# Kernel tuning notes

Hardware: AMD Instinct MI355X
Metric: run time of the kernel (lower is better)

## Reference

```python
import jax, jax.numpy as jnp
import numpy as np

B, CIN, H, W = 4, 272, 32, 32
D, NHEAD, DFF, E, TOPK, NDEC = 256, 8, 1024, 8, 2, 2
HW = H * W


def _sine_pos():
    npf = D // 2
    ye = jnp.cumsum(jnp.ones((H, W), jnp.float32), 0)
    xe = jnp.cumsum(jnp.ones((H, W), jnp.float32), 1)
    eps, scale = 1e-6, 2.0 * np.pi
    ye = ye / (ye[-1:, :] + eps) * scale
    xe = xe / (xe[:, -1:] + eps) * scale
    t = jnp.arange(npf, dtype=jnp.float32)
    dim_t = 10000.0 ** (2.0 * jnp.floor(t / 2.0) / npf)
    px = xe[:, :, None] / dim_t
    py = ye[:, :, None] / dim_t
    px = jnp.stack((jnp.sin(px[:, :, 0::2]), jnp.cos(px[:, :, 1::2])), axis=3).reshape(H, W, npf)
    py = jnp.stack((jnp.sin(py[:, :, 0::2]), jnp.cos(py[:, :, 1::2])), axis=3).reshape(H, W, npf)
    return jnp.concatenate((py, px), axis=2).reshape(HW, D)


def _ln(v, g, b):
    m = v.mean(-1, keepdims=True)
    var = ((v - m) ** 2).mean(-1, keepdims=True)
    return (v - m) / jnp.sqrt(var + 1e-5) * g + b


def _mha(q_in, k_in, v_in, Wqkv, bqkv, Wo, bo):
    # seq-first [S,B,D], torch nn.MultiheadAttention math (dropout off)
    S = q_in.shape[0]; T = k_in.shape[0]; dh = D // NHEAD
    Wq, Wk, Wv = jnp.split(Wqkv, 3, 0)
    bq, bk, bv = jnp.split(bqkv, 3)
    q = (q_in @ Wq.T + bq).reshape(S, B, NHEAD, dh)
    k = (k_in @ Wk.T + bk).reshape(T, B, NHEAD, dh)
    v = (v_in @ Wv.T + bv).reshape(T, B, NHEAD, dh)
    attn = jax.nn.softmax(jnp.einsum('sbhd,tbhd->bhst', q, k) / np.sqrt(dh), axis=-1)
    o = jnp.einsum('bhst,tbhd->sbhd', attn, v).reshape(S, B, D)
    return o @ Wo.T + bo


def _moe(xt, Wg, bg, W1, b1, W2, b2):
    # FMoETransformerMLP with NaiveGate: top-k gate, per-expert 2-layer MLP, weighted combine
    S = xt.shape[0]
    xf = xt.reshape(-1, D)
    N = xf.shape[0]
    logits = xf @ Wg.T + bg                              # [N, E]
    topv, topi = jax.lax.top_k(logits, TOPK)             # [N, k]
    score = jax.nn.softmax(topv, axis=-1)                # softmax over selected logits
    comb = jnp.zeros((N, E), xf.dtype).at[jnp.arange(N)[:, None], topi].add(score)
    h = jax.nn.relu(jnp.einsum('nd,edh->neh', xf, W1) + b1)   # [N, E, DFF]
    y = jnp.einsum('neh,ehd->ned', h, W2) + b2                # [N, E, D]
    out = jnp.einsum('ne,ned->nd', comb, y)
    return out.reshape(S, B, D)


def setup_inputs() -> dict:
    key = jax.random.key(0)
    ks = iter(jax.random.split(key, 32))
    g = lambda shp, s=0.02: s * jax.random.normal(next(ks), shp, jnp.float32)
    inp = {
        'x': jax.random.normal(next(ks), (B, CIN, H, W), jnp.float32),
        'Wi': g((D, CIN)), 'bi': jnp.zeros((D,), jnp.float32),
        'learned_embed': g((HW, D), 1.0),
        'Wqkv_s': g((3 * D, D)), 'bqkv_s': jnp.zeros((3 * D,), jnp.float32),
        'Wo_s': g((D, D)), 'bo_s': jnp.zeros((D,), jnp.float32),
        'Wqkv_c': g((3 * D, D)), 'bqkv_c': jnp.zeros((3 * D,), jnp.float32),
        'Wo_c': g((D, D)), 'bo_c': jnp.zeros((D,), jnp.float32),
        'ln_g': jnp.ones((4 * NDEC, D), jnp.float32), 'ln_b': jnp.zeros((4 * NDEC, D), jnp.float32),
        'gate_w1': g((E, D)), 'gate_b1': jnp.zeros((E,), jnp.float32),
        'W1a': g((E, D, DFF)), 'b1a': jnp.zeros((E, DFF), jnp.float32),
        'W2a': g((E, DFF, D)), 'b2a': jnp.zeros((E, D), jnp.float32),
        'gate_w2': g((E, D)), 'gate_b2': jnp.zeros((E,), jnp.float32),
        'W1b': g((E, D, DFF)), 'b1b': jnp.zeros((E, DFF), jnp.float32),
        'W2b': g((E, DFF, D)), 'b2b': jnp.zeros((E, D), jnp.float32),
        'Wout': g((CIN, D)), 'bout': jnp.zeros((CIN,), jnp.float32),
    }
    return inp


def reference(x, Wi, bi, learned_embed, Wqkv_s, bqkv_s, Wo_s, bo_s,
              Wqkv_c, bqkv_c, Wo_c, bo_c, ln_g, ln_b,
              gate_w1, gate_b1, W1a, b1a, W2a, b2a,
              gate_w2, gate_b2, W1b, b1b, W2b, b2b, Wout, bout):
    tokens = x.transpose(2, 3, 0, 1).reshape(HW, B, CIN)   # 'b c h w -> (h w) b c'
    src = tokens @ Wi.T + bi                               # input_proj
    pos = _sine_pos()[:, None, :]                          # [HW,1,D] broadcast over batch
    enc = src
    dec = src
    for i in range(NDEC):
        tgt = jnp.broadcast_to(learned_embed[:, None, :], (HW, B, D))
        t2 = _mha(tgt + pos, enc + pos, enc, Wqkv_s, bqkv_s, Wo_s, bo_s)
        tgt = _ln(tgt + t2, ln_g[4 * i], ln_b[4 * i])
        t2 = _mha(tgt + pos, dec + pos, dec, Wqkv_c, bqkv_c, Wo_c, bo_c)
        tgt = _ln(tgt + t2, ln_g[4 * i + 1], ln_b[4 * i + 1])
        od = tgt + _moe(tgt, gate_w1, gate_b1, W1a, b1a, W2a, b2a)   # post-lnorm: residual only
        od = _ln(od, ln_g[4 * i + 2], ln_b[4 * i + 2])
        od = od + _moe(od, gate_w2, gate_b2, W1b, b1b, W2b, b2b)
        dec = _ln(od, ln_g[4 * i + 3], ln_b[4 * i + 3])
    rec = dec @ Wout.T + bout                              # output_proj, [HW,B,CIN]
    feature_rec = rec.reshape(H, W, B, CIN).transpose(2, 3, 0, 1)
    return feature_rec
```

## Files before the change

kernel.cpp:

```cpp
#include <hip/hip_runtime.h>

#define NHW 1024
#define NB 4
#define DM 256
#define NTOK 4096
#define NCIN 272
#define NDFF 1024

typedef unsigned short u16;
typedef unsigned int u32;
typedef __attribute__((ext_vector_type(8))) short s16x8;
typedef __attribute__((ext_vector_type(4))) float f32x4;

static const int GEMM_SMEM32 = (32+32+64+64)*56*2;
static const int GEMM_SMEM64 = (32+32+64+64)*72*2;

__device__ __forceinline__ float4 ld4(const float* p){ return *(const float4*)p; }
__device__ __forceinline__ void st4(float* p, float4 v){ *(float4*)p = v; }

__device__ __forceinline__ void splitf(float x, u16& h, u16& l){
  u32 u = __float_as_uint(x);
  u32 hu = (u + (0x7FFFu + ((u >> 16) & 1u))) >> 16;
  h = (u16)hu;
  float hf = __uint_as_float(hu << 16);
  float r = x - hf;
  u32 v = __float_as_uint(r);
  v += 0x7FFFu + ((v >> 16) & 1u);
  l = (u16)(v >> 16);
}

__device__ __forceinline__ u32 packf(float x){
  u16 h,l; splitf(x,h,l);
  return (u32)h | ((u32)l << 16);
}

__global__ void pos_kernel(float* __restrict__ pos){
  int s = blockIdx.x, d = threadIdx.x;
  int row = s >> 5, col = s & 31;
  float base = (d < 128) ? (float)(row + 1) : (float)(col + 1);
  float val = base / (32.0f + 1e-6f) * 6.2831853071795864f;
  int dd = (d < 128) ? d : d - 128;
  int mf = dd >> 1;
  float f = powf(10000.0f, (float)mf * (1.0f/64.0f));
  float a = val / f;
  pos[s*DM + d] = (dd & 1) ? cosf(a) : sinf(a);
}

__global__ void tin_kernel(const float* __restrict__ x, float* __restrict__ tok){
  int idx = blockIdx.x*256 + threadIdx.x;
  if (idx >= NTOK*NCIN) return;
  int c = idx % NCIN;
  int n = idx / NCIN;
  int s = n >> 2, b = n & 3;
  tok[idx] = x[((long)(b*NCIN + c))*NHW + s];
}
__global__ void tout_kernel(const float* __restrict__ rec, float* __restrict__ out){
  int idx = blockIdx.x*256 + threadIdx.x;
  if (idx >= NTOK*NCIN) return;
  int s = idx & (NHW-1);
  int bc = idx >> 10;
  int b = bc / NCIN, c = bc % NCIN;
  out[idx] = rec[((long)(s*NB + b))*NCIN + c];
}

__global__ __launch_bounds__(256) void tconv_kernel(const float* __restrict__ in,
    u16* __restrict__ oh, u16* __restrict__ ol, int K, int N){
  __shared__ float tile[32][33];
  long base = (long)blockIdx.z * (long)K * (long)N;
  int k0 = blockIdx.y*32, n0 = blockIdx.x*32;
  int tx = threadIdx.x & 31, ty = threadIdx.x >> 5;
  #pragma unroll
  for (int i=0;i<32;i+=8)
    tile[ty+i][tx] = in[base + (long)(k0+ty+i)*N + n0+tx];
  __syncthreads();
  #pragma unroll
  for (int i=0;i<32;i+=8){
    float v = tile[tx][ty+i];
    u16 h,l; splitf(v,h,l);
    long o = base + (long)(n0+ty+i)*K + k0+tx;
    oh[o]=h; ol[o]=l;
  }
}

__global__ void wsplit_kernel(const float* __restrict__ in, u16* __restrict__ oh,
    u16* __restrict__ ol, int n){
  int i = blockIdx.x*256 + threadIdx.x;
  if (i < n){ u16 h,l; splitf(in[i],h,l); oh[i]=h; ol[i]=l; }
}

template<bool GROUPED, bool INDIRECT, int ASRC, bool RELU, int CDST, int BK>
__device__ __forceinline__ void sgemm_body(
    const void* __restrict__ Av, int lda,
    const float* __restrict__ pos,
    const u16* __restrict__ Bhp, const u16* __restrict__ Blp, int ldb,
    const float* __restrict__ bias,
    void* __restrict__ Cv, int ldc,
    int M, int N, int K,
    const int* __restrict__ map,
    const int* __restrict__ cnt,
    const int* __restrict__ offs,
    const int* __restrict__ jmap,
    const float* __restrict__ sflat,
    long strideB, int strideBias, int e)
{
  constexpr int BM = 32;
  constexpr int NSEG = BK/32;
  constexpr int SW = (BK==32) ? 56 : 72;
  int rows = GROUPED ? cnt[e] : M;
  int bn = blockIdx.x, bm = blockIdx.y;
  if (bm*BM >= rows) return;
  int row0 = GROUPED ? offs[e] : 0;
  const float* Af = (const float*)Av;
  const u32*   Ap = (const u32*)Av;
  if (GROUPED){ Bhp += (long)e*strideB; Blp += (long)e*strideB; }
  const float* biasp = bias ? (GROUPED ? bias + (long)e*strideBias : bias) : nullptr;

  extern __shared__ u16 smem[];
  u16* Ah = smem;
  u16* Al = Ah + BM*SW;
  u16* Bh = Al + BM*SW;
  u16* Bl = Bh + 64*SW;

  int tid = threadIdx.x;
  int w = tid >> 6, ln = tid & 63;
  int wm = w >> 1, wn = w & 1;
  int lr = ln & 15, lh = ln >> 4;
  int srow = tid >> 2, sseg = tid & 3;

  int bgrow = bn*64 + srow;
  bool bok = bgrow < N;
  int agrow = bm*BM + srow;
  bool aok = (tid < BM*4) && (agrow < rows);
  long arow = 0;
  if (aok) arow = INDIRECT ? (long)map[row0 + agrow] : (long)(row0 + agrow);

  const f32x4 z4 = {0.f,0.f,0.f,0.f};
  f32x4 acc0 = z4, acc1 = z4;
  const s16x8 z8 = {0,0,0,0,0,0,0,0};

  s16x8 rBh[NSEG], rBl[NSEG];
  uint4 rA0[NSEG], rA1[NSEG];
  float4 rP0[NSEG], rP1[NSEG];

  auto load_stage = [&](int k0){
    #pragma unroll
    for (int s=0; s<NSEG; s++){
      int kk = k0 + s*32 + sseg*8;
      bool kok = kk < K;
      rBh[s] = z8; rBl[s] = z8;
      if (bok && kok){
        rBh[s] = *(const s16x8*)&Bhp[(long)bgrow*ldb + kk];
        rBl[s] = *(const s16x8*)&Blp[(long)bgrow*ldb + kk];
      }
      if (tid < BM*4){
        rA0[s] = make_uint4(0,0,0,0); rA1[s] = make_uint4(0,0,0,0);
        if (ASRC==2 || ASRC==3){ rP0[s] = make_float4(0.f,0.f,0.f,0.f); rP1[s] = rP0[s]; }
        if (aok && kok){
          if (ASRC == 1){
            rA0[s] = *(const uint4*)&Ap[arow*lda + kk];
            rA1[s] = *(const uint4*)&Ap[arow*lda + kk + 4];
          } else {
            long aoff = (ASRC==3 ? (long)(arow>>2) : arow)*lda + kk;
            rA0[s] = *(const uint4*)&Af[aoff];
            rA1[s] = *(const uint4*)&Af[aoff + 4];
            if (ASRC==2 || ASRC==3){
              long poff = (long)(arow>>2)*DM + kk;
              rP0[s] = ld4(&pos[poff]);
              rP1[s] = ld4(&pos[poff + 4]);
            }
          }
        }
      }
    }
  };

  auto write_stage = [&](){
    #pragma unroll
    for (int s=0; s<NSEG; s++){
      *(s16x8*)&Bh[srow*SW + s*32 + sseg*8] = rBh[s];
      *(s16x8*)&Bl[srow*SW + s*32 + sseg*8] = rBl[s];
      if (tid < BM*4){
        s16x8 hv, lv;
        if (ASRC == 1){
          u32 ws[8] = {rA0[s].x,rA0[s].y,rA0[s].z,rA0[s].w,rA1[s].x,rA1[s].y,rA1[s].z,rA1[s].w};
          #pragma unroll
          for (int t=0;t<8;t++){ hv[t]=(short)(ws[t]&0xFFFFu); lv[t]=(short)(ws[t]>>16); }
        } else {
          float xs[8] = {__uint_as_float(rA0[s].x),__uint_as_float(rA0[s].y),
                         __uint_as_float(rA0[s].z),__uint_as_float(rA0[s].w),
                         __uint_as_float(rA1[s].x),__uint_as_float(rA1[s].y),
                         __uint_as_float(rA1[s].z),__uint_as_float(rA1[s].w)};
          if (ASRC==2 || ASRC==3){
            xs[0]+=rP0[s].x; xs[1]+=rP0[s].y; xs[2]+=rP0[s].z; xs[3]+=rP0[s].w;
            xs[4]+=rP1[s].x; xs[5]+=rP1[s].y; xs[6]+=rP1[s].z; xs[7]+=rP1[s].w;
          }
          #pragma unroll
          for (int t=0;t<8;t++){ u16 hh,ll; splitf(xs[t],hh,ll); hv[t]=(short)hh; lv[t]=(short)ll; }
        }
        *(s16x8*)&Ah[srow*SW + s*32 + sseg*8] = hv;
        *(s16x8*)&Al[srow*SW + s*32 + sseg*8] = lv;
      }
    }
  };

  load_stage(0);
  for (int k0 = 0; k0 < K; k0 += BK){
    write_stage();
    __syncthreads();
    if (k0 + BK < K) load_stage(k0 + BK);
    #pragma unroll
    for (int s=0; s<NSEG; s++){
      int co = s*32 + lh*8;
      s16x8 a0h = *(const s16x8*)&Ah[(wm*16 + lr)*SW + co];
      s16x8 a0l = *(const s16x8*)&Al[(wm*16 + lr)*SW + co];
      s16x8 b0h = *(const s16x8*)&Bh[(wn*32      + lr)*SW + co];
      s16x8 b1h = *(const s16x8*)&Bh[(wn*32 + 16 + lr)*SW + co];
      s16x8 b0l = *(const s16x8*)&Bl[(wn*32      + lr)*SW + co];
      s16x8 b1l = *(const s16x8*)&Bl[(wn*32 + 16 + lr)*SW + co];
      acc0 = __builtin_amdgcn_mfma_f32_16x16x32_bf16(a0h, b0h, acc0, 0,0,0);
      acc1 = __builtin_amdgcn_mfma_f32_16x16x32_bf16(a0h, b1h, acc1, 0,0,0);
      acc0 = __builtin_amdgcn_mfma_f32_16x16x32_bf16(a0h, b0l, acc0, 0,0,0);
      acc1 = __builtin_amdgcn_mfma_f32_16x16x32_bf16(a0h, b1l, acc1, 0,0,0);
      acc0 = __builtin_amdgcn_mfma_f32_16x16x32_bf16(a0l, b0h, acc0, 0,0,0);
      acc1 = __builtin_amdgcn_mfma_f32_16x16x32_bf16(a0l, b1h, acc1, 0,0,0);
    }
    __syncthreads();
  }

  int c0 = bn*64 + wn*32 + lr;
  int c1 = c0 + 16;
  float bv0 = (biasp && c0 < N) ? biasp[c0] : 0.f;
  float bv1 = (biasp && c1 < N) ? biasp[c1] : 0.f;
  int rbase = bm*BM + wm*16 + lh*4;
  auto stc = [&](int gr, int gc, float vv){
    if (gr < rows && gc < N){
      float t = RELU ? fmaxf(vv, 0.f) : vv;
      if (CDST == 1){
        ((u32*)Cv)[(long)(row0+gr)*ldc + gc] = packf(t);
      } else if (CDST == 2){
        int ts = jmap[row0+gr];
        ((float*)Cv)[(long)ts*ldc + gc] = t * sflat[ts];
      } else {
        ((float*)Cv)[(long)(row0+gr)*ldc + gc] = t;
      }
    }
  };
  #pragma unroll
  for (int r = 0; r < 4; r++){
    stc(rbase + r, c0, acc0[r] + bv0);
    stc(rbase + r, c1, acc1[r] + bv1);
  }
}

__global__ __launch_bounds__(256) void gemm_in(const float* A, const u16* Bh_, const u16* Bl_,
    const float* bias, float* C){
  sgemm_body<false,false,0,false,0,32>(A, NCIN, nullptr, Bh_, Bl_, NCIN, bias, C, DM,
      NTOK, DM, NCIN, nullptr, nullptr, nullptr, nullptr, nullptr, 0, 0, 0);
}

__global__ __launch_bounds__(256) void gemm_out_k(const float* A, const u16* Bh_, const u16* Bl_,
    const float* bias, float* C){
  sgemm_body<false,false,0,false,0,32>(A, DM, nullptr, Bh_, Bl_, DM, bias, C, NCIN,
      NTOK, NCIN, DM, nullptr, nullptr, nullptr, nullptr, nullptr, 0, 0, 0);
}

__global__ __launch_bounds__(256) void gemm_wos(const u32* A, const u16* Bh_, const u16* Bl_,
    const float* bias, float* C){
  sgemm_body<false,false,1,false,0,32>(A, DM, nullptr, Bh_, Bl_, DM, bias, C, DM,
      NTOK, DM, DM, nullptr, nullptr, nullptr, nullptr, nullptr, 0, 0, 0);
}

__global__ __launch_bounds__(256) void gemm_woc(const u32* A, const u16* Bh_, const u16* Bl_,
    const float* bias, float* C){
  sgemm_body<false,false,1,false,0,32>(A, DM, nullptr, Bh_, Bl_, DM, bias, C, DM,
      NTOK, DM, DM, nullptr, nullptr, nullptr, nullptr, nullptr, 0, 0, 0);
}

template<int MQ, int MK>
__device__ __forceinline__ void qkv_body(const float* Aq, const float* Ak, const float* Avv,
    const float* pos, const u16* Bwh, const u16* Bwl, const float* bias,
    u32* Cq, u32* Ck, u32* Cvv){
  int z = blockIdx.z;
  const float* A = z==0 ? Aq : (z==1 ? Ak : Avv);
  u32* C = z==0 ? Cq : (z==1 ? Ck : Cvv);
  const u16* Bph = Bwh + (long)z*256*DM;
  const u16* Bpl = Bwl + (long)z*256*DM;
  const float* bp = bias + z*256;
  int mode = z==0 ? MQ : (z==1 ? MK : 0);
  if (mode == 3)
    sgemm_body<false,false,3,false,1,32>(A, DM, pos, Bph, Bpl, DM, bp, C, DM,
        NTOK, DM, DM, nullptr, nullptr, nullptr, nullptr, nullptr, 0, 0, 0);
  else if (mode == 2)
    sgemm_body<false,false,2,false,1,32>(A, DM, pos, Bph, Bpl, DM, bp, C, DM,
        NTOK, DM, DM, nullptr, nullptr, nullptr, nullptr, nullptr, 0, 0, 0);
  else
    sgemm_body<false,false,0,false,1,32>(A, DM, pos, Bph, Bpl, DM, bp, C, DM,
        NTOK, DM, DM, nullptr, nullptr, nullptr, nullptr, nullptr, 0, 0, 0);
}

__global__ __launch_bounds__(256) void gemm_qkv_s(const float* Aq, const float* Ak,
    const float* Avv, const float* pos, const u16* Bwh, const u16* Bwl, const float* bias,
    u32* Cq, u32* Ck, u32* Cvv){
  qkv_body<3,2>(Aq, Ak, Avv, pos, Bwh, Bwl, bias, Cq, Ck, Cvv);
}
__global__ __launch_bounds__(256) void gemm_qkv_c(const float* Aq, const float* Ak,
    const float* Avv, const float* pos, const u16* Bwh, const u16* Bwl, const float* bias,
    u32* Cq, u32* Ck, u32* Cvv){
  qkv_body<2,2>(Aq, Ak, Avv, pos, Bwh, Bwl, bias, Cq, Ck, Cvv);
}

__global__ __launch_bounds__(256) void gemm_m1(const float* A, const u16* Bh_, const u16* Bl_,
    const float* bias, u32* C, const int* map, const int* cnt, const int* offs){
  sgemm_body<true,true,0,true,1,32>(A, DM, nullptr, Bh_, Bl_, DM, bias, C, NDFF,
      0, NDFF, DM, map, cnt, offs, nullptr, nullptr, 262144L, NDFF, blockIdx.z);
}

__global__ __launch_bounds__(256) void gemm_m2(const u32* A, const u16* Bh_, const u16* Bl_,
    const float* bias, float* C, const int* cnt, const int* offs,
    const int* jmap, const float* sflat){
  sgemm_body<true,false,1,false,2,64>(A, NDFF, nullptr, Bh_, Bl_, NDFF, bias, C, DM,
      0, DM, NDFF, nullptr, cnt, offs, jmap, sflat, 262144L, DM, blockIdx.z);
}

__global__ __launch_bounds__(256) void attn_mfma(const u32* __restrict__ Q,
    const u32* __restrict__ Kb, const u32* __restrict__ Vb, u32* __restrict__ O)
{
  __shared__ u16 Kh[64*40], Kl[64*40];
  __shared__ u16 Vh[32*72], Vl[32*72];
  __shared__ u16 Ph[4][16*72], Pl[4][16*72];

  int qt = blockIdx.x, bh = blockIdx.y;
  int b = bh >> 3, h = bh & 7;
  int tid = threadIdx.x;
  int wv = tid >> 6, ln = tid & 63;
  int lr = ln & 15, lh = ln >> 4;
  const float scale = 0.17677669529663687f;

  s16x8 qh, ql;
  {
    long qrow = ((long)((qt*64 + wv*16 + lr)*NB + b))*DM + h*32 + lh*8;
    uint4 p0 = *(const uint4*)&Q[qrow];
    uint4 p1 = *(const uint4*)&Q[qrow + 4];
    u32 ws[8] = {p0.x,p0.y,p0.z,p0.w,p1.x,p1.y,p1.z,p1.w};
    #pragma unroll
    for (int t=0;t<8;t++){ qh[t]=(short)(ws[t]&0xFFFFu); ql[t]=(short)(ws[t]>>16); }
  }

  int skey = tid >> 2, soct = tid & 3;
  int vkey0 = tid >> 3,        vd0 = (tid & 7) << 2;
  int vkey1 = (tid + 256) >> 3, vd1 = ((tid + 256) & 7) << 2;

  uint4 rK0, rK1, rV0, rV1;

  auto load_kv = [&](int kt){
    long gk = ((long)((kt*64 + skey)*NB + b))*DM + h*32 + soct*8;
    rK0 = *(const uint4*)&Kb[gk];
    rK1 = *(const uint4*)&Kb[gk + 4];
    rV0 = *(const uint4*)&Vb[((long)((kt*64 + vkey0)*NB + b))*DM + h*32 + vd0];
    rV1 = *(const uint4*)&Vb[((long)((kt*64 + vkey1)*NB + b))*DM + h*32 + vd1];
  };

  auto write_kv = [&](){
    u32 ws[8] = {rK0.x,rK0.y,rK0.z,rK0.w,rK1.x,rK1.y,rK1.z,rK1.w};
    s16x8 hv, lv;
    #pragma unroll
    for (int t=0;t<8;t++){ hv[t]=(short)(ws[t]&0xFFFFu); lv[t]=(short)(ws[t]>>16); }
    *(s16x8*)&Kh[skey*40 + soct*8] = hv;
    *(s16x8*)&Kl[skey*40 + soct*8] = lv;
    u32 v0[4] = {rV0.x,rV0.y,rV0.z,rV0.w};
    u32 v1[4] = {rV1.x,rV1.y,rV1.z,rV1.w};
    #pragma unroll
    for (int t=0;t<4;t++){
      Vh[(vd0+t)*72 + vkey0] = (u16)(v0[t]&0xFFFFu);
      Vl[(vd0+t)*72 + vkey0] = (u16)(v0[t]>>16);
      Vh[(vd1+t)*72 + vkey1] = (u16)(v1[t]&0xFFFFu);
      Vl[(vd1+t)*72 + vkey1] = (u16)(v1[t]>>16);
    }
  };

  const f32x4 z4 = {0.f,0.f,0.f,0.f};
  f32x4 oacc0 = z4, oacc1 = z4;
  float m[4]  = {-1e30f,-1e30f,-1e30f,-1e30f};
  float lp[4] = {0.f,0.f,0.f,0.f};

  load_kv(0);
  for (int kt = 0; kt < 16; kt++){
    write_kv();
    __syncthreads();
    if (kt + 1 < 16) load_kv(kt + 1);

    f32x4 sacc[4];
    #pragma unroll
    for (int s16t=0; s16t<4; s16t++){
      s16x8 kbh = *(const s16x8*)&Kh[(s16t*16 + lr)*40 + lh*8];
      s16x8 kbl = *(const s16x8*)&Kl[(s16t*16 + lr)*40 + lh*8];
      f32x4 a = z4;
      a = __builtin_amdgcn_mfma_f32_16x16x32_bf16(qh, kbh, a, 0,0,0);
      a = __builtin_amdgcn_mfma_f32_16x16x32_bf16(qh, kbl, a, 0,0,0);
      a = __builtin_amdgcn_mfma_f32_16x16x32_bf16(ql, kbh, a, 0,0,0);
      a[0]*=scale; a[1]*=scale; a[2]*=scale; a[3]*=scale;
      sacc[s16t] = a;
    }
    float tm[4];
    #pragma unroll
    for (int r=0;r<4;r++)
      tm[r] = fmaxf(fmaxf(sacc[0][r],sacc[1][r]), fmaxf(sacc[2][r],sacc[3][r]));
    #pragma unroll
    for (int mask=1; mask<=8; mask<<=1){
      #pragma unroll
      for (int r=0;r<4;r++) tm[r] = fmaxf(tm[r], __shfl_xor(tm[r], mask));
    }
    #pragma unroll
    for (int r=0;r<4;r++){
      float mn = fmaxf(m[r], tm[r]);
      float al = __expf(m[r] - mn);
      m[r] = mn;
      lp[r] *= al;
      oacc0[r] *= al;
      oacc1[r] *= al;
    }
    #pragma unroll
    for (int s16t=0; s16t<4; s16t++){
      #pragma unroll
      for (int r=0;r<4;r++){
        float p = __expf(sacc[s16t][r] - m[r]);
        lp[r] += p;
        u16 hh,ll; splitf(p,hh,ll);
        int off = (lh*4 + r)*72 + s16t*16 + lr;
        Ph[wv][off] = hh;
        Pl[wv][off] = ll;
      }
    }
    #pragma unroll
    for (int ks=0; ks<2; ks++){
      s16x8 pah = *(const s16x8*)&Ph[wv][lr*72 + ks*32 + lh*8];
      s16x8 pal = *(const s16x8*)&Pl[wv][lr*72 + ks*32 + lh*8];
      s16x8 vh0 = *(const s16x8*)&Vh[lr*72      + ks*32 + lh*8];
      s16x8 vl0 = *(const s16x8*)&Vl[lr*72      + ks*32 + lh*8];
      s16x8 vh1 = *(const s16x8*)&Vh[(16+lr)*72 + ks*32 + lh*8];
      s16x8 vl1 = *(const s16x8*)&Vl[(16+lr)*72 + ks*32 + lh*8];
      oacc0 = __builtin_amdgcn_mfma_f32_16x16x32_bf16(pah, vh0, oacc0, 0,0,0);
      oacc0 = __builtin_amdgcn_mfma_f32_16x16x32_bf16(pah, vl0, oacc0, 0,0,0);
      oacc0 = __builtin_amdgcn_mfma_f32_16x16x32_bf16(pal, vh0, oacc0, 0,0,0);
      oacc1 = __builtin_amdgcn_mfma_f32_16x16x32_bf16(pah, vh1, oacc1, 0,0,0);
      oacc1 = __builtin_amdgcn_mfma_f32_16x16x32_bf16(pah, vl1, oacc1, 0,0,0);
      oacc1 = __builtin_amdgcn_mfma_f32_16x16x32_bf16(pal, vh1, oacc1, 0,0,0);
    }
    __syncthreads();
  }
  #pragma unroll
  for (int mask=1; mask<=8; mask<<=1){
    #pragma unroll
    for (int r=0;r<4;r++) lp[r] += __shfl_xor(lp[r], mask);
  }
  #pragma unroll
  for (int r=0;r<4;r++){
    float inv = 1.f/lp[r];
    int q = qt*64 + wv*16 + lh*4 + r;
    long orow = ((long)(q*NB + b))*DM + h*32;
    O[orow + lr]      = packf(oacc0[r]*inv);
    O[orow + 16 + lr] = packf(oacc1[r]*inv);
  }
}

__device__ __forceinline__ float wave_sum(float v){
  #pragma unroll
  for (int m=1; m<64; m<<=1) v += __shfl_xor(v, m);
  return v;
}

__device__ __forceinline__ float4 ln_finish(float4 a, const float* g, const float* beta, int lane){
  float sum = wave_sum(a.x+a.y+a.z+a.w);
  float sq  = wave_sum(a.x*a.x + a.y*a.y + a.z*a.z + a.w*a.w);
  float mean = sum * (1.f/DM);
  float var  = sq * (1.f/DM) - mean*mean;
  float inv = 1.0f / sqrtf(var + 1e-5f);
  float4 gg = ld4(&g[lane*4]);
  float4 bb = ld4(&beta[lane*4]);
  float4 ov;
  ov.x = (a.x-mean)*inv*gg.x + bb.x;
  ov.y = (a.y-mean)*inv*gg.y + bb.y;
  ov.z = (a.z-mean)*inv*gg.z + bb.z;
  ov.w = (a.w-mean)*inv*gg.w + bb.w;
  return ov;
}

__device__ __forceinline__ void gate_from_regs(float4 ov, int row, int lane,
    const float* GW, const float* GB, float* scores, int* topi){
  float lg[8];
  #pragma unroll
  for (int e=0; e<8; e++){
    float4 wv = ld4(&GW[e*DM + lane*4]);
    lg[e] = ov.x*wv.x + ov.y*wv.y + ov.z*wv.z + ov.w*wv.w;
  }
  #pragma unroll
  for (int mask=1; mask<64; mask<<=1){
    #pragma unroll
    for (int e=0; e<8; e++) lg[e] += __shfl_xor(lg[e], mask);
  }
  #pragma unroll
  for (int e=0; e<8; e++) lg[e] += GB[e];
  int i0 = 0; float v0 = lg[0];
  #pragma unroll
  for (int e=1; e<8; e++) if (lg[e] > v0){ v0 = lg[e]; i0 = e; }
  int i1 = -1; float v1 = -1e30f;
  #pragma unroll
  for (int e=0; e<8; e++) if (e != i0 && lg[e] > v1){ v1 = lg[e]; i1 = e; }
  if (lane == 0){
    float ee = expf(v1 - v0);
    float inv = 1.f/(1.f + ee);
    scores[row*2]   = inv;
    scores[row*2+1] = ee*inv;
    topi[row*2]   = i0;
    topi[row*2+1] = i1;
  }
}

__global__ __launch_bounds__(256) void add_ln_le(const float* __restrict__ A,
    const float* __restrict__ Bv, const float* __restrict__ g, const float* __restrict__ beta,
    float* __restrict__ out)
{
  int row = blockIdx.x*4 + (threadIdx.x >> 6);
  int lane = threadIdx.x & 63;
  float4 a = ld4(&A[(long)(row>>2)*DM + lane*4]);
  float4 b = ld4(&Bv[(long)row*DM + lane*4]);
  a.x+=b.x; a.y+=b.y; a.z+=b.z; a.w+=b.w;
  float4 ov = ln_finish(a, g, beta, lane);
  st4(&out[(long)row*DM + lane*4], ov);
}

__global__ __launch_bounds__(256) void add_ln_gate(const float* __restrict__ A,
    const float* __restrict__ Bv, const float* __restrict__ g, const float* __restrict__ beta,
    float* __restrict__ out, const float* __restrict__ GW, const float* __restrict__ GB,
    float* __restrict__ scores, int* __restrict__ topi)
{
  int row = blockIdx.x*4 + (threadIdx.x >> 6);
  int lane = threadIdx.x & 63;
  float4 a = ld4(&A[(long)row*DM + lane*4]);
  float4 b = ld4(&Bv[(long)row*DM + lane*4]);
  a.x+=b.x; a.y+=b.y; a.z+=b.z; a.w+=b.w;
  float4 ov = ln_finish(a, g, beta, lane);
  st4(&out[(long)row*DM + lane*4], ov);
  gate_from_regs(ov, row, lane, GW, GB, scores, topi);
}

__global__ __launch_bounds__(256) void moe_ln_gate_k(const float* __restrict__ base,
    const float* __restrict__ yt,
    const float* __restrict__ g, const float* __restrict__ beta, float* __restrict__ out,
    const float* __restrict__ GW, const float* __restrict__ GB,
    float* __restrict__ scores2, int* __restrict__ topi2)
{
  int row = blockIdx.x*4 + (threadIdx.x >> 6);
  int lane = threadIdx.x & 63;
  float4 a  = ld4(&base[(long)row*DM + lane*4]);
  float4 y0 = ld4(&yt[(long)(row*2)*DM + lane*4]);
  float4 y1 = ld4(&yt[(long)(row*2+1)*DM + lane*4]);
  a.x += y0.x + y1.x;
  a.y += y0.y + y1.y;
  a.z += y0.z + y1.z;
  a.w += y0.w + y1.w;
  float4 ov = ln_finish(a, g, beta, lane);
  st4(&out[(long)row*DM + lane*4], ov);
  gate_from_regs(ov, row, lane, GW, GB, scores2, topi2);
}

__global__ __launch_bounds__(256) void moe_ln_fin_k(const float* __restrict__ base,
    const float* __restrict__ yt,
    const float* __restrict__ g, const float* __restrict__ beta, float* __restrict__ out)
{
  int row = blockIdx.x*4 + (threadIdx.x >> 6);
  int lane = threadIdx.x & 63;
  float4 a  = ld4(&base[(long)row*DM + lane*4]);
  float4 y0 = ld4(&yt[(long)(row*2)*DM + lane*4]);
  float4 y1 = ld4(&yt[(long)(row*2+1)*DM + lane*4]);
  a.x += y0.x + y1.x;
  a.y += y0.y + y1.y;
  a.z += y0.z + y1.z;
  a.w += y0.w + y1.w;
  float4 ov = ln_finish(a, g, beta, lane);
  st4(&out[(long)row*DM + lane*4], ov);
}

__global__ void offs_assign(const int* __restrict__ topi, int* __restrict__ cnt_g,
    int* __restrict__ offs_g, int* __restrict__ map, int* __restrict__ jmap)
{
  __shared__ int hist[72];
  __shared__ int offs[8];
  __shared__ int c2[8];
  int tid = threadIdx.x;
  if (tid < 72) hist[tid] = 0;
  __syncthreads();
  for (int idx = tid; idx < 2*NTOK; idx += 256){
    int e = topi[idx];
    atomicAdd(&hist[e*9 + (tid & 7)], 1);
  }
  __syncthreads();
  if (tid == 0){
    int o = 0;
    #pragma unroll
    for (int e=0; e<8; e++){
      int c = 0;
      #pragma unroll
      for (int s=0; s<8; s++) c += hist[e*9 + s];
      cnt_g[e] = c;
      offs[e] = o;
      offs_g[e] = o;
      o += c;
      c2[e] = 0;
    }
  }
  __syncthreads();
  for (int n = tid; n < NTOK; n += 256){
    #pragma unroll
    for (int j=0; j<2; j++){
      int e = topi[n*2+j];
      int slot = atomicAdd(&c2[e], 1);
      int r = offs[e] + slot;
      map[r] = n;
      jmap[r] = n*2 + j;
    }
  }
}

extern "C" void kernel_launch(void* const* d_in, const int* in_sizes, int n_in,
                              void* d_out, int out_size, void* d_ws, size_t ws_size,
                              hipStream_t stream)
{
  const float* x      = (const float*)d_in[0];
  const float* Wi     = (const float*)d_in[1];
  const float* bi     = (const float*)d_in[2];
  const float* le     = (const float*)d_in[3];
  const float* Wqkv_s = (const float*)d_in[4];
  const float* bqkv_s = (const float*)d_in[5];
  const float* Wo_s   = (const float*)d_in[6];
  const float* bo_s   = (const float*)d_in[7];
  const float* Wqkv_c = (const float*)d_in[8];
  const float* bqkv_c = (const float*)d_in[9];
  const float* Wo_c   = (const float*)d_in[10];
  const float* bo_c   = (const float*)d_in[11];
  const float* ln_g   = (const float*)d_in[12];
  const float* ln_b   = (const float*)d_in[13];
  const float* gw1    = (const float*)d_in[14];
  const float* gb1    = (const float*)d_in[15];
  const float* W1a    = (const float*)d_in[16];
  const float* b1a    = (const float*)d_in[17];
  const float* W2a    = (const float*)d_in[18];
  const float* b2a    = (const float*)d_in[19];
  const float* gw2    = (const float*)d_in[20];
  const float* gb2    = (const float*)d_in[21];
  const float* W1b    = (const float*)d_in[22];
  const float* b1b    = (const float*)d_in[23];
  const float* W2b    = (const float*)d_in[24];
  const float* b2b    = (const float*)d_in[25];
  const float* Wout   = (const float*)d_in[26];
  const float* bout   = (const float*)d_in[27];

  float* w = (float*)d_ws;
  const long SZ = 1048576;
  float* pos  = w;
  float* src  = pos  + 262144;
  float* t2s  = src  + SZ;
  float* tgtA = t2s  + SZ;
  float* dec  = tgtA + SZ;
  float* od   = dec;
  float* od2  = dec  + SZ;
  float* yt   = od2  + SZ;
  float* scoresA = yt + 2097152;
  float* scoresB = scoresA + 8192;
  u16* wsp  = (u16*)(scoresB + 8192);
  u16* W1ah = wsp;             u16* W1al = wsp + 2097152;
  u16* W1bh = wsp + 4194304;   u16* W1bl = wsp + 6291456;
  u16* W2ah = wsp + 8388608;   u16* W2al = wsp + 10485760;
  u16* W2bh = wsp + 12582912;  u16* W2bl = wsp + 14680064;
  u16* dwp  = wsp + 16777216;
  u16* Wih   = dwp;            u16* Wil   = dwp + 69632;
  u16* Wqsh  = dwp + 139264;   u16* Wqsl  = dwp + 335872;
  u16* Wosh  = dwp + 532480;   u16* Wosl  = dwp + 598016;
  u16* Wqch  = dwp + 663552;   u16* Wqcl  = dwp + 860160;
  u16* Woch  = dwp + 1056768;  u16* Wocl  = dwp + 1122304;
  u16* Wouth = dwp + 1187840;  u16* Woutl = dwp + 1257472;
  float* R   = (float*)(dwp + 1327104);
  float* tok = R;
  u32*  q    = (u32*)R;
  u32*  k    = (u32*)(R + SZ);
  u32*  v    = (u32*)(R + 2*SZ);
  u32*  ao   = (u32*)(R + 3*SZ);
  u32*  hg   = (u32*)R;
  float* rec = R;
  int* ip    = (int*)(R + 8388608);
  int* topiA = ip;
  int* topiB = ip + 8192;
  int* map   = ip + 16384;
  int* jmapA = ip + 24576;
  int* jmapB = ip + 32768;
  int* cnts  = ip + 40960;
  int* offsg = ip + 40992;

  dim3 blk(256);
  dim3 gDense(4, 128, 1);
  dim3 gQKV(4, 128, 3);
  dim3 gMoe1(16, 128, 8);
  dim3 gMoe2(4, 128, 8);
  dim3 gAttn(16, 32);

  pos_kernel<<<NHW, DM, 0, stream>>>(pos);
  tin_kernel<<<(NTOK*NCIN + 255)/256, blk, 0, stream>>>(x, tok);

  tconv_kernel<<<dim3(32, 8, 8), blk, 0, stream>>>(W1a, W1ah, W1al, DM,   NDFF);
  tconv_kernel<<<dim3(32, 8, 8), blk, 0, stream>>>(W1b, W1bh, W1bl, DM,   NDFF);
  tconv_kernel<<<dim3(8, 32, 8), blk, 0, stream>>>(W2a, W2ah, W2al, NDFF, DM);
  tconv_kernel<<<dim3(8, 32, 8), blk, 0, stream>>>(W2b, W2bh, W2bl, NDFF, DM);
  wsplit_kernel<<<272, blk, 0, stream>>>(Wi,     Wih,   Wil,   69632);
  wsplit_kernel<<<768, blk, 0, stream>>>(Wqkv_s, Wqsh,  Wqsl,  196608);
  wsplit_kernel<<<256, blk, 0, stream>>>(Wo_s,   Wosh,  Wosl,  65536);
  wsplit_kernel<<<768, blk, 0, stream>>>(Wqkv_c, Wqch,  Wqcl,  196608);
  wsplit_kernel<<<256, blk, 0, stream>>>(Wo_c,   Woch,  Wocl,  65536);
  wsplit_kernel<<<272, blk, 0, stream>>>(Wout,   Wouth, Woutl, 69632);

  gemm_in<<<gDense, blk, GEMM_SMEM32, stream>>>(tok, Wih, Wil, bi, src);

  gemm_qkv_s<<<gQKV, blk, GEMM_SMEM32, stream>>>(le, src, src, pos, Wqsh, Wqsl, bqkv_s, q, k, v);
  attn_mfma<<<gAttn, blk, 0, stream>>>(q, k, v, ao);
  gemm_wos<<<gDense, blk, GEMM_SMEM32, stream>>>(ao, Wosh, Wosl, bo_s, t2s);

  const float* decIn = src;
  for (int i = 0; i < 2; i++){
    int* cntA = cnts + (i*2)*8;   int* offsA = offsg + (i*2)*8;
    int* cntB = cnts + (i*2+1)*8; int* offsB = offsg + (i*2+1)*8;

    add_ln_le<<<1024, blk, 0, stream>>>(le, t2s, ln_g + (4*i)*DM, ln_b + (4*i)*DM, tgtA);
    gemm_qkv_c<<<gQKV, blk, GEMM_SMEM32, stream>>>(tgtA, decIn, decIn, pos, Wqch, Wqcl, bqkv_c, q, k, v);
    attn_mfma<<<gAttn, blk, 0, stream>>>(q, k, v, ao);
    gemm_woc<<<gDense, blk, GEMM_SMEM32, stream>>>(ao, Woch, Wocl, bo_c, (float*)k);
    add_ln_gate<<<1024, blk, 0, stream>>>(tgtA, (float*)k, ln_g + (4*i+1)*DM, ln_b + (4*i+1)*DM, od,
        gw1, gb1, scoresA, topiA);

    offs_assign<<<1, blk, 0, stream>>>(topiA, cntA, offsA, map, jmapA);
    gemm_m1<<<gMoe1, blk, GEMM_SMEM32, stream>>>(od, W1ah, W1al, b1a, hg, map, cntA, offsA);
    gemm_m2<<<gMoe2, blk, GEMM_SMEM64, stream>>>(hg, W2ah, W2al, b2a, yt, cntA, offsA,
        jmapA, scoresA);
    moe_ln_gate_k<<<1024, blk, 0, stream>>>(od, yt,
        ln_g + (4*i+2)*DM, ln_b + (4*i+2)*DM, od2, gw2, gb2, scoresB, topiB);

    offs_assign<<<1, blk, 0, stream>>>(topiB, cntB, offsB, map, jmapB);
    gemm_m1<<<gMoe1, blk, GEMM_SMEM32, stream>>>(od2, W1bh, W1bl, b1b, hg, map, cntB, offsB);
    gemm_m2<<<gMoe2, blk, GEMM_SMEM64, stream>>>(hg, W2bh, W2bl, b2b, yt, cntB, offsB,
        jmapB, scoresB);
    moe_ln_fin_k<<<1024, blk, 0, stream>>>(od2, yt,
        ln_g + (4*i+3)*DM, ln_b + (4*i+3)*DM, dec);

    decIn = dec;
  }

  gemm_out_k<<<dim3(5,128,1), blk, GEMM_SMEM32, stream>>>(dec, Wouth, Woutl, bout, rec);
  tout_kernel<<<(NTOK*NCIN + 255)/256, blk, 0, stream>>>(rec, (float*)d_out);
}
```

Baseline: 640.9 us.

## Split attention over key dimension into two halves with a merge kernel

```diff
diff --git a/kernel.cpp b/kernel.cpp
--- a/kernel.cpp
+++ b/kernel.cpp
@@ -323,18 +323,23 @@
 }
 
 __global__ __launch_bounds__(256) void attn_mfma(const u32* __restrict__ Q,
-    const u32* __restrict__ Kb, const u32* __restrict__ Vb, u32* __restrict__ O)
+    const u32* __restrict__ Kb, const u32* __restrict__ Vb,
+    float* __restrict__ OpBase, float* __restrict__ mBase, float* __restrict__ lBase)
 {
   __shared__ u16 Kh[64*40], Kl[64*40];
   __shared__ u16 Vh[32*72], Vl[32*72];
   __shared__ u16 Ph[4][16*72], Pl[4][16*72];
 
-  int qt = blockIdx.x, bh = blockIdx.y;
+  int qt = blockIdx.x, bh = blockIdx.y, z = blockIdx.z;
   int b = bh >> 3, h = bh & 7;
   int tid = threadIdx.x;
   int wv = tid >> 6, ln = tid & 63;
   int lr = ln & 15, lh = ln >> 4;
   const float scale = 0.17677669529663687f;
+  int kt0 = z*8, kt1 = z*8 + 8;
+  float* Op   = OpBase + (long)z*NTOK*DM;
+  float* mArr = mBase + (long)z*65536;
+  float* lArr = lBase + (long)z*65536;
 
   s16x8 qh, ql;
   {
@@ -383,11 +388,11 @@
   float m[4]  = {-1e30f,-1e30f,-1e30f,-1e30f};
   float lp[4] = {0.f,0.f,0.f,0.f};
 
-  load_kv(0);
-  for (int kt = 0; kt < 16; kt++){
+  load_kv(kt0);
+  for (int kt = kt0; kt < kt1; kt++){
     write_kv();
     __syncthreads();
-    if (kt + 1 < 16) load_kv(kt + 1);
+    if (kt + 1 < kt1) load_kv(kt + 1);
 
     f32x4 sacc[4];
     #pragma unroll
@@ -455,12 +460,38 @@
   }
   #pragma unroll
   for (int r=0;r<4;r++){
-    float inv = 1.f/lp[r];
     int q = qt*64 + wv*16 + lh*4 + r;
-    long orow = ((long)(q*NB + b))*DM + h*32;
-    O[orow + lr]      = packf(oacc0[r]*inv);
-    O[orow + 16 + lr] = packf(oacc1[r]*inv);
-  }
+    long n = (long)q*NB + b;
+    long orow = n*DM + h*32;
+    Op[orow + lr]      = oacc0[r];
+    Op[orow + 16 + lr] = oacc1[r];
+    if (lr == 0){
+      mArr[n*8 + h] = m[r];
+      lArr[n*8 + h] = lp[r];
+    }
+  }
+}
+
+__global__ __launch_bounds__(256) void attn_merge(const float* __restrict__ OpBase,
+    const float* __restrict__ mBase, const float* __restrict__ lBase, u32* __restrict__ ao)
+{
+  int gid = blockIdx.x*256 + threadIdx.x;
+  int n = gid >> 6;
+  int d4 = (gid & 63) << 2;
+  int h = d4 >> 5;
+  int nh = n*8 + h;
+  float m0 = mBase[nh], l0 = lBase[nh];
+  float m1 = mBase[65536 + nh], l1 = lBase[65536 + nh];
+  float M = fmaxf(m0, m1);
+  float w0 = __expf(m0 - M), w1 = __expf(m1 - M);
+  float inv = 1.f / (w0*l0 + w1*l1);
+  long o = (long)n*DM + d4;
+  float4 a = ld4(&OpBase[o]);
+  float4 c = ld4(&OpBase[(long)NTOK*DM + o]);
+  ao[o+0] = packf((w0*a.x + w1*c.x)*inv);
+  ao[o+1] = packf((w0*a.y + w1*c.y)*inv);
+  ao[o+2] = packf((w0*a.z + w1*c.z)*inv);
+  ao[o+3] = packf((w0*a.w + w1*c.w)*inv);
 }
 
 __device__ __forceinline__ float wave_sum(float v){
@@ -685,6 +716,9 @@
   u32*  k    = (u32*)(R + SZ);
   u32*  v    = (u32*)(R + 2*SZ);
   u32*  ao   = (u32*)(R + 3*SZ);
+  float* OpB = R + 4*SZ;
+  float* mB  = R + 6*SZ;
+  float* lB  = mB + 131072;
   u32*  hg   = (u32*)R;
   float* rec = R;
   int* ip    = (int*)(R + 8388608);
@@ -701,7 +735,7 @@
   dim3 gQKV(4, 128, 3);
   dim3 gMoe1(16, 128, 8);
   dim3 gMoe2(4, 128, 8);
-  dim3 gAttn(16, 32);
+  dim3 gAttn(16, 32, 2);
 
   pos_kernel<<<NHW, DM, 0, stream>>>(pos);
   tin_kernel<<<(NTOK*NCIN + 255)/256, blk, 0, stream>>>(x, tok);
@@ -720,7 +754,8 @@
   gemm_in<<<gDense, blk, GEMM_SMEM32, stream>>>(tok, Wih, Wil, bi, src);
 
   gemm_qkv_s<<<gQKV, blk, GEMM_SMEM32, stream>>>(le, src, src, pos, Wqsh, Wqsl, bqkv_s, q, k, v);
-  attn_mfma<<<gAttn, blk, 0, stream>>>(q, k, v, ao);
+  attn_mfma<<<gAttn, blk, 0, stream>>>(q, k, v, OpB, mB, lB);
+  attn_merge<<<1024, blk, 0, stream>>>(OpB, mB, lB, ao);
   gemm_wos<<<gDense, blk, GEMM_SMEM32, stream>>>(ao, Wosh, Wosl, bo_s, t2s);
 
   const float* decIn = src;
@@ -730,7 +765,8 @@
 
     add_ln_le<<<1024, blk, 0, stream>>>(le, t2s, ln_g + (4*i)*DM, ln_b + (4*i)*DM, tgtA);
     gemm_qkv_c<<<gQKV, blk, GEMM_SMEM32, stream>>>(tgtA, decIn, decIn, pos, Wqch, Wqcl, bqkv_c, q, k, v);
-    attn_mfma<<<gAttn, blk, 0, stream>>>(q, k, v, ao);
+    attn_mfma<<<gAttn, blk, 0, stream>>>(q, k, v, OpB, mB, lB);
+    attn_merge<<<1024, blk, 0, stream>>>(OpB, mB, lB, ao);
     gemm_woc<<<gDense, blk, GEMM_SMEM32, stream>>>(ao, Woch, Wocl, bo_c, (float*)k);
     add_ln_gate<<<1024, blk, 0, stream>>>(tgtA, (float*)k, ln_g + (4*i+1)*DM, ln_b + (4*i+1)*DM, od,
         gw1, gb1, scoresA, topiA);
```

New measurement: 635.7 us. No clear change (-0.8%).
